# Kernel optimization log

Measured on AMD Instinct MI355X. Metric: run time of the kernel, lower is better.

Reference implementation:

```python
import jax, jax.numpy as jnp
import numpy as np

B = 4096       # batch of instance features
N = 131072     # num_samples (cluster memory slots)
D = 256        # num_features
TEMP = 0.05
EPS = 1e-12    # F.normalize eps


def setup_inputs() -> dict:
    key = jax.random.key(0)
    k1, k2, k3 = jax.random.split(key, 3)
    inputs = jax.random.normal(k1, (B, D), dtype=jnp.float32)
    targets = jax.random.randint(k2, (B,), 0, N, dtype=jnp.int64)
    # learned/buffer memory bank; original registers zeros but is populated with
    # L2-normalized cluster centroids before use -> initialize likewise
    feats = jax.random.normal(k3, (N, D), dtype=jnp.float32)
    feats = feats / jnp.linalg.norm(feats, axis=1, keepdims=True)
    feature_memory = jnp.zeros((1,), dtype=jnp.float32)  # unused by forward
    return {"inputs": inputs, "targets": targets, "feature_memory": feature_memory,
            "k": 10, "features": feats}


def reference(inputs, targets, feature_memory, k, features):
    # inputs: [B, D], targets: [B] int, features: [N, D]
    # F.normalize(inputs, dim=1)
    nrm = jnp.linalg.norm(inputs, axis=1, keepdims=True)
    x = inputs / jnp.maximum(nrm, EPS)
    # CM_Hard forward output: x @ features.T  (the per-cluster argmin loop has
    # no effect on the forward output; it only drives the buffer EMA in backward)
    logits = jnp.matmul(x, features.T) / TEMP          # [B, N]
    # F.cross_entropy(logits, targets), mean reduction
    lse = jax.nn.logsumexp(logits, axis=1)             # [B]
    tgt_logit = jnp.take_along_axis(logits, targets[:, None].astype(jnp.int32), axis=1)[:, 0]
    loss = jnp.mean(lse - tgt_logit)
    return loss
```

## Files before the change

### kernel.cpp

```cpp
#include <hip/hip_runtime.h>
#include <hip/hip_bf16.h>


typedef __attribute__((ext_vector_type(8))) short bf16x8;
typedef __attribute__((ext_vector_type(4))) float f32x4;
typedef __attribute__((address_space(1))) unsigned int u32g;
typedef __attribute__((address_space(3))) unsigned int u32l;

#define B_ROWS   4096
#define N_FEATS  131072
#define D_DIM    256
#define SCALE_B2 28.853900817779268f
#define LN2F     0.69314718055994531f

#define BM 128
#define BN 128
#define BKT 64
#define NCHUNK 32
#define COLS_PB (N_FEATS / NCHUNK)
#define NTILES  (COLS_PB / BN)
#define TILE_B  (BN * BKT * 2)
#define NSLICE  (NCHUNK * 4)

#define E2(x) __builtin_amdgcn_exp2f(x)

static __device__ __forceinline__ unsigned short f2bf(float x) {
    __hip_bfloat16 h = __float2bfloat16(x);
    return __builtin_bit_cast(unsigned short, h);
}
static __device__ __forceinline__ float bf2f(unsigned short u) {
    return __builtin_bit_cast(float, ((unsigned int)u) << 16);
}

__global__ __launch_bounds__(64) void k_normalize(const float* __restrict__ in,
                                                  unsigned short* __restrict__ xb) {
    const int row  = blockIdx.x;
    const int lane = threadIdx.x;
    float4 v = *(const float4*)(in + (size_t)row * D_DIM + lane * 4);
    float ss = v.x * v.x + v.y * v.y + v.z * v.z + v.w * v.w;
#pragma unroll
    for (int mask = 1; mask < 64; mask <<= 1) ss += __shfl_xor(ss, mask);
    const float sc = SCALE_B2 / fmaxf(sqrtf(ss), 1e-12f);
    ushort4 o;
    o.x = f2bf(v.x * sc); o.y = f2bf(v.y * sc);
    o.z = f2bf(v.z * sc); o.w = f2bf(v.w * sc);
    *(ushort4*)(xb + (size_t)row * D_DIM + lane * 4) = o;
}

__global__ __launch_bounds__(256) void k_cvt_feats(const float* __restrict__ f,
                                                   unsigned short* __restrict__ fb) {
    const int total4 = N_FEATS * D_DIM / 4;
    const int stride = gridDim.x * blockDim.x;
    for (int i = blockIdx.x * blockDim.x + threadIdx.x; i < total4; i += stride) {
        float4 v = ((const float4*)f)[i];
        ushort4 o;
        o.x = f2bf(v.x); o.y = f2bf(v.y); o.z = f2bf(v.z); o.w = f2bf(v.w);
        ((ushort4*)fb)[i] = o;
    }
}

#define STAGE(t_, buf_) do {                                                          \
        const int nt_ = (t_) >> 2, kt_ = (t_) & 3;                                    \
        const unsigned short* s_ = fb + (nbase + (size_t)nt_ * BN) * D_DIM + kt_ * BKT; \
        char* d_ = &Bs[(buf_) * TILE_B + dBase];                                      \
        __builtin_amdgcn_global_load_lds((const u32g*)(s_ + e0), (u32l*)d_, 16, 0, 0);\
        __builtin_amdgcn_global_load_lds((const u32g*)(s_ + e1), (u32l*)(d_ + 8192), 16, 0, 0); \
    } while (0)

#define COMPUTE(ktL, bufL) do {                                                       \
        const char* buf_ = &Bs[(bufL) * TILE_B];                                      \
        bf16x8 bfr[2][2];                                                             \
        _Pragma("unroll")                                                             \
        for (int ks2 = 0; ks2 < 2; ++ks2)                                             \
        _Pragma("unroll")                                                             \
            for (int n = 0; n < 2; ++n) {                                             \
                const int col = wc * 32 + n * 16 + l15;                               \
                const int off = (col * 128 + ks2 * 64 + l4 * 16) ^ ((col & 7) << 4);  \
                bfr[ks2][n] = *(const bf16x8*)(buf_ + off);                           \
            }                                                                         \
        __builtin_amdgcn_s_setprio(1);                                                \
        _Pragma("unroll")                                                             \
        for (int ks2 = 0; ks2 < 2; ++ks2)                                             \
        _Pragma("unroll")                                                             \
            for (int m = 0; m < 4; ++m)                                               \
        _Pragma("unroll")                                                             \
                for (int n = 0; n < 2; ++n)                                           \
                    acc[m][n] = __builtin_amdgcn_mfma_f32_16x16x32_bf16(              \
                        afr[m][(ktL) * 2 + ks2], bfr[ks2][n], acc[m][n], 0, 0, 0);    \
        __builtin_amdgcn_s_setprio(0);                                                \
    } while (0)

#define EPI() do {                                                                    \
        _Pragma("unroll")                                                             \
        for (int m = 0; m < 4; ++m)                                                   \
        _Pragma("unroll")                                                             \
            for (int j = 0; j < 4; ++j) {                                             \
                const int r = m * 4 + j;                                              \
                s_run[r] += E2(acc[m][0][j]) + E2(acc[m][1][j]);                      \
            }                                                                         \
        _Pragma("unroll")                                                             \
        for (int m = 0; m < 4; ++m)                                                   \
        _Pragma("unroll")                                                             \
            for (int n = 0; n < 2; ++n) acc[m][n] = (f32x4){0.f, 0.f, 0.f, 0.f};      \
    } while (0)

#define LOADCVT(t_) do {                                                              \
        const int nt_ = (t_) >> 2, kt_ = (t_) & 3;                                    \
        const float* s0_ = featf + (nbase + (size_t)nt_ * BN + fc0) * D_DIM + kt_ * BKT + fk0; \
        const float* s1_ = featf + (nbase + (size_t)nt_ * BN + fc1) * D_DIM + kt_ * BKT + fk1; \
        float4 a0 = *(const float4*)s0_, a1 = *(const float4*)(s0_ + 4);              \
        float4 b0 = *(const float4*)s1_, b1 = *(const float4*)(s1_ + 4);              \
        unsigned short ua[8] = {f2bf(a0.x), f2bf(a0.y), f2bf(a0.z), f2bf(a0.w),       \
                                f2bf(a1.x), f2bf(a1.y), f2bf(a1.z), f2bf(a1.w)};      \
        unsigned short ub[8] = {f2bf(b0.x), f2bf(b0.y), f2bf(b0.z), f2bf(b0.w),       \
                                f2bf(b1.x), f2bf(b1.y), f2bf(b1.z), f2bf(b1.w)};      \
        ra = *(int4*)ua; rb = *(int4*)ub;                                             \
    } while (0)
#define WRITEB(buf_) do {                                                             \
        char* d_ = &Bs[(buf_) * TILE_B];                                              \
        *(int4*)(d_ + wo0) = ra;                                                      \
        *(int4*)(d_ + wo1) = rb;                                                      \
    } while (0)

template <bool BF16B>
__global__ __launch_bounds__(512, 2) void k_lse_gemm(
    const unsigned short* __restrict__ xb,
    const float* __restrict__ featf,
    const unsigned short* __restrict__ fb,
    float* __restrict__ partials)
{
    __shared__ char Bs[4 * TILE_B];

    const int hw  = blockIdx.y * 32 + blockIdx.x;
    const int lid = (hw & 7) * 128 + (hw >> 3);
    const int bx  = lid & 31;
    const int by  = lid >> 5;

    const int tid  = threadIdx.x;
    const int lane = tid & 63;
    const int w    = tid >> 6;
    const int wr   = w >> 2;
    const int wc   = w & 3;
    const int l15  = lane & 15;
    const int l4   = lane >> 4;

    const int brow     = bx * BM;
    const size_t nbase = (size_t)by * COLS_PB;

    bf16x8 afr[4][8];
#pragma unroll
    for (int m = 0; m < 4; ++m) {
        const unsigned short* ap =
            xb + (size_t)(brow + wr * 64 + m * 16 + l15) * D_DIM + l4 * 8;
#pragma unroll
        for (int ks = 0; ks < 8; ++ks)
            afr[m][ks] = *(const bf16x8*)(ap + ks * 32);
    }

    f32x4 acc[4][2];
#pragma unroll
    for (int m = 0; m < 4; ++m)
#pragma unroll
        for (int n = 0; n < 2; ++n) acc[m][n] = (f32x4){0.f, 0.f, 0.f, 0.f};
    float s_run[16];
#pragma unroll
    for (int r = 0; r < 16; ++r) s_run[r] = 0.f;

    if (BF16B) {
        int e0, e1;
        {
            const int p0 = w * 1024 + lane * 16;
            const int c0 = p0 >> 7;
            e0 = c0 * D_DIM + ((((p0 ^ ((c0 & 7) << 4)) >> 4) & 7) * 8);
            const int p1 = p0 + 8192;
            const int c1 = p1 >> 7;
            e1 = c1 * D_DIM + ((((p1 ^ ((c1 & 7) << 4)) >> 4) & 7) * 8);
        }
        const int dBase = w * 1024;

        STAGE(0, 0);
        STAGE(1, 1);
        for (int nt = 0; nt < NTILES; ++nt) {
            STAGE(nt * 4 + 2, 2);
            asm volatile("s_waitcnt vmcnt(4)\ns_barrier" ::: "memory");
            COMPUTE(0, 0);
            STAGE(nt * 4 + 3, 3);
            asm volatile("s_waitcnt vmcnt(4)\ns_barrier" ::: "memory");
            COMPUTE(1, 1);
            if (nt < NTILES - 1) {
                STAGE(nt * 4 + 4, 0);
                asm volatile("s_waitcnt vmcnt(4)\ns_barrier" ::: "memory");
            } else {
                asm volatile("s_waitcnt vmcnt(2)\ns_barrier" ::: "memory");
            }
            COMPUTE(2, 2);
            if (nt < NTILES - 1) {
                STAGE(nt * 4 + 5, 1);
                asm volatile("s_waitcnt vmcnt(4)\ns_barrier" ::: "memory");
            } else {
                asm volatile("s_waitcnt vmcnt(0)\ns_barrier" ::: "memory");
            }
            COMPUTE(3, 3);
            EPI();
        }
    } else {
        const int c0 = tid, c1 = tid + 512;
        const int fc0 = c0 >> 3, fk0 = (c0 & 7) * 8;
        const int fc1 = c1 >> 3, fk1 = (c1 & 7) * 8;
        const int wo0 = (fc0 * 128 + fk0 * 2) ^ ((fc0 & 7) << 4);
        const int wo1 = (fc1 * 128 + fk1 * 2) ^ ((fc1 & 7) << 4);
        int4 ra, rb;
        LOADCVT(0); WRITEB(0);
        __syncthreads();
        for (int nt = 0; nt < NTILES; ++nt) {
            { LOADCVT(nt * 4 + 1); COMPUTE(0, 0); WRITEB(1); __syncthreads(); }
            { LOADCVT(nt * 4 + 2); COMPUTE(1, 1); WRITEB(0); __syncthreads(); }
            { LOADCVT(nt * 4 + 3); COMPUTE(2, 0); WRITEB(1); __syncthreads(); }
            {
                if (nt < NTILES - 1) LOADCVT(nt * 4 + 4);
                COMPUTE(3, 1);
                EPI();
                if (nt < NTILES - 1) { WRITEB(0); }
                __syncthreads();
            }
        }
    }

#pragma unroll
    for (int r = 0; r < 16; ++r) {
        float S = s_run[r];
#pragma unroll
        for (int mask = 1; mask < 16; mask <<= 1) S += __shfl_xor(S, mask);
        s_run[r] = S;
    }
    if (l15 == 0) {
        const int slice = by * 4 + wc;
#pragma unroll
        for (int r = 0; r < 16; ++r) {
            const int m = r >> 2, j = r & 3;
            const int row = brow + wr * 64 + m * 16 + l4 * 4 + j;
            partials[(size_t)row * NSLICE + slice] = s_run[r];
        }
    }
}

__global__ __launch_bounds__(64) void k_finalize(const float* __restrict__ partials,
                                                 const unsigned short* __restrict__ xb,
                                                 const float* __restrict__ feats,
                                                 const int* __restrict__ targets,
                                                 float* __restrict__ loss) {
    const int row  = blockIdx.x;
    const int lane = threadIdx.x;
    float S = partials[(size_t)row * NSLICE + lane]
            + partials[(size_t)row * NSLICE + 64 + lane];

    const int t = targets[row];
    ushort4 xv = *(const ushort4*)(xb + (size_t)row * D_DIM + lane * 4);
    float4  fv = *(const float4*)(feats + (size_t)t * D_DIM + lane * 4);
    float dot = bf2f(xv.x) * fv.x + bf2f(xv.y) * fv.y +
                bf2f(xv.z) * fv.z + bf2f(xv.w) * fv.w;
#pragma unroll
    for (int mask = 1; mask < 64; mask <<= 1) {
        S   += __shfl_xor(S, mask);
        dot += __shfl_xor(dot, mask);
    }
    if (lane == 0) loss[row] = LN2F * (__builtin_amdgcn_logf(S) - dot);
}

__global__ __launch_bounds__(256) void k_reduce(const float* __restrict__ loss,
                                                float* __restrict__ out) {
    __shared__ float sm[4];
    const int tid = threadIdx.x;
    float s = 0.f;
    for (int i = tid; i < B_ROWS; i += 256) s += loss[i];
#pragma unroll
    for (int mask = 1; mask < 64; mask <<= 1) s += __shfl_xor(s, mask);
    if ((tid & 63) == 0) sm[tid >> 6] = s;
    __syncthreads();
    if (tid == 0) out[0] = (sm[0] + sm[1] + sm[2] + sm[3]) * (1.0f / B_ROWS);
}

extern "C" void kernel_launch(void* const* d_in, const int* in_sizes, int n_in,
                              void* d_out, int out_size, void* d_ws, size_t ws_size,
                              hipStream_t stream) {
    const float* inputs  = (const float*)d_in[0];
    const int*   targets = (const int*)d_in[1];
    const float* feats   = (const float*)d_in[4];
    float* out = (float*)d_out;

    char* ws = (char*)d_ws;
    const size_t off_xb       = 0;
    const size_t off_partials = off_xb + (size_t)B_ROWS * D_DIM * 2;
    const size_t off_loss     = off_partials + (size_t)B_ROWS * NSLICE * sizeof(float);
    const size_t off_fb       = off_loss + (size_t)B_ROWS * sizeof(float);
    const size_t need_fb      = off_fb + (size_t)N_FEATS * D_DIM * 2;

    unsigned short* xb = (unsigned short*)(ws + off_xb);
    float* partials    = (float*)(ws + off_partials);
    float* loss        = (float*)(ws + off_loss);
    unsigned short* fb = (unsigned short*)(ws + off_fb);
    const bool precvt  = ws_size >= need_fb;

    k_normalize<<<B_ROWS, 64, 0, stream>>>(inputs, xb);
    if (precvt) {
        k_cvt_feats<<<2048, 256, 0, stream>>>(feats, fb);
        k_lse_gemm<true><<<dim3(32, NCHUNK), 512, 0, stream>>>(xb, feats, fb, partials);
    } else {
        k_lse_gemm<false><<<dim3(32, NCHUNK), 512, 0, stream>>>(xb, feats, fb, partials);
    }
    k_finalize<<<B_ROWS, 64, 0, stream>>>(partials, xb, feats, targets, loss);
    k_reduce<<<1, 256, 0, stream>>>(loss, out);
}
```

Baseline: 285.9 us.

## Widen GEMM N-tile to 256 and cut column chunks to 8

Doubles the per-block N tile from 128 to 256 columns. Each wave now computes a 64x64 output tile, so every loaded A fragment feeds twice as many MFMAs. The column chunk count drops from 32 to 8, giving fewer partial slices for the finalize kernel, and the block swizzle becomes a simple row/column split. The trade-offs are doubled LDS use (4 buffers of 32KB, 128KB per block), twice the accumulator registers, and possibly lower occupancy under launch_bounds(512,2).

```diff
diff --git a/kernel.cpp b/kernel.cpp
--- a/kernel.cpp
+++ b/kernel.cpp
@@ -14,9 +14,9 @@
 #define LN2F     0.69314718055994531f
 
 #define BM 128
-#define BN 128
+#define BN 256
 #define BKT 64
-#define NCHUNK 32
+#define NCHUNK 8
 #define COLS_PB (N_FEATS / NCHUNK)
 #define NTILES  (COLS_PB / BN)
 #define TILE_B  (BN * BKT * 2)
@@ -65,16 +65,18 @@
         char* d_ = &Bs[(buf_) * TILE_B + dBase];                                      \
         __builtin_amdgcn_global_load_lds((const u32g*)(s_ + e0), (u32l*)d_, 16, 0, 0);\
         __builtin_amdgcn_global_load_lds((const u32g*)(s_ + e1), (u32l*)(d_ + 8192), 16, 0, 0); \
+        __builtin_amdgcn_global_load_lds((const u32g*)(s_ + e2), (u32l*)(d_ + 16384), 16, 0, 0); \
+        __builtin_amdgcn_global_load_lds((const u32g*)(s_ + e3), (u32l*)(d_ + 24576), 16, 0, 0); \
     } while (0)
 
 #define COMPUTE(ktL, bufL) do {                                                       \
         const char* buf_ = &Bs[(bufL) * TILE_B];                                      \
-        bf16x8 bfr[2][2];                                                             \
+        bf16x8 bfr[2][4];                                                             \
         _Pragma("unroll")                                                             \
         for (int ks2 = 0; ks2 < 2; ++ks2)                                             \
         _Pragma("unroll")                                                             \
-            for (int n = 0; n < 2; ++n) {                                             \
-                const int col = wc * 32 + n * 16 + l15;                               \
+            for (int n = 0; n < 4; ++n) {                                             \
+                const int col = wc * 64 + n * 16 + l15;                               \
                 const int off = (col * 128 + ks2 * 64 + l4 * 16) ^ ((col & 7) << 4);  \
                 bfr[ks2][n] = *(const bf16x8*)(buf_ + off);                           \
             }                                                                         \
@@ -84,7 +86,7 @@
         _Pragma("unroll")                                                             \
             for (int m = 0; m < 4; ++m)                                               \
         _Pragma("unroll")                                                             \
-                for (int n = 0; n < 2; ++n)                                           \
+                for (int n = 0; n < 4; ++n)                                           \
                     acc[m][n] = __builtin_amdgcn_mfma_f32_16x16x32_bf16(              \
                         afr[m][(ktL) * 2 + ks2], bfr[ks2][n], acc[m][n], 0, 0, 0);    \
         __builtin_amdgcn_s_setprio(0);                                                \
@@ -96,30 +98,32 @@
         _Pragma("unroll")                                                             \
             for (int j = 0; j < 4; ++j) {                                             \
                 const int r = m * 4 + j;                                              \
-                s_run[r] += E2(acc[m][0][j]) + E2(acc[m][1][j]);                      \
+                s_run[r] += (E2(acc[m][0][j]) + E2(acc[m][1][j]))                     \
+                          + (E2(acc[m][2][j]) + E2(acc[m][3][j]));                    \
             }                                                                         \
         _Pragma("unroll")                                                             \
         for (int m = 0; m < 4; ++m)                                                   \
         _Pragma("unroll")                                                             \
-            for (int n = 0; n < 2; ++n) acc[m][n] = (f32x4){0.f, 0.f, 0.f, 0.f};      \
-    } while (0)
-
-#define LOADCVT(t_) do {                                                              \
-        const int nt_ = (t_) >> 2, kt_ = (t_) & 3;                                    \
-        const float* s0_ = featf + (nbase + (size_t)nt_ * BN + fc0) * D_DIM + kt_ * BKT + fk0; \
-        const float* s1_ = featf + (nbase + (size_t)nt_ * BN + fc1) * D_DIM + kt_ * BKT + fk1; \
-        float4 a0 = *(const float4*)s0_, a1 = *(const float4*)(s0_ + 4);              \
-        float4 b0 = *(const float4*)s1_, b1 = *(const float4*)(s1_ + 4);              \
-        unsigned short ua[8] = {f2bf(a0.x), f2bf(a0.y), f2bf(a0.z), f2bf(a0.w),       \
-                                f2bf(a1.x), f2bf(a1.y), f2bf(a1.z), f2bf(a1.w)};      \
-        unsigned short ub[8] = {f2bf(b0.x), f2bf(b0.y), f2bf(b0.z), f2bf(b0.w),       \
-                                f2bf(b1.x), f2bf(b1.y), f2bf(b1.z), f2bf(b1.w)};      \
-        ra = *(int4*)ua; rb = *(int4*)ub;                                             \
-    } while (0)
+            for (int n = 0; n < 4; ++n) acc[m][n] = (f32x4){0.f, 0.f, 0.f, 0.f};      \
+    } while (0)
+
+#define LOADCVT1(q_, t_, r_) do {                                                     \
+        const int cc_ = tid + (q_) * 512;                                             \
+        const int col_ = cc_ >> 3, k_ = (cc_ & 7) * 8;                                \
+        const float* s_ = featf + (nbase + (size_t)((t_) >> 2) * BN + col_) * D_DIM   \
+                          + ((t_) & 3) * BKT + k_;                                    \
+        float4 f0 = *(const float4*)s_;                                               \
+        float4 f1 = *(const float4*)(s_ + 4);                                         \
+        unsigned short u_[8] = {f2bf(f0.x), f2bf(f0.y), f2bf(f0.z), f2bf(f0.w),       \
+                                f2bf(f1.x), f2bf(f1.y), f2bf(f1.z), f2bf(f1.w)};      \
+        r_ = *(int4*)u_;                                                              \
+    } while (0)
+#define LOADCVT(t_) do { LOADCVT1(0, t_, ra); LOADCVT1(1, t_, rb);                    \
+                         LOADCVT1(2, t_, rc); LOADCVT1(3, t_, rd); } while (0)
 #define WRITEB(buf_) do {                                                             \
         char* d_ = &Bs[(buf_) * TILE_B];                                              \
-        *(int4*)(d_ + wo0) = ra;                                                      \
-        *(int4*)(d_ + wo1) = rb;                                                      \
+        *(int4*)(d_ + wo0) = ra; *(int4*)(d_ + wo1) = rb;                             \
+        *(int4*)(d_ + wo2) = rc; *(int4*)(d_ + wo3) = rd;                             \
     } while (0)
 
 template <bool BF16B>
@@ -132,9 +136,8 @@
     __shared__ char Bs[4 * TILE_B];
 
     const int hw  = blockIdx.y * 32 + blockIdx.x;
-    const int lid = (hw & 7) * 128 + (hw >> 3);
-    const int bx  = lid & 31;
-    const int by  = lid >> 5;
+    const int bx  = hw >> 3;
+    const int by  = hw & 7;
 
     const int tid  = threadIdx.x;
     const int lane = tid & 63;
@@ -157,17 +160,17 @@
             afr[m][ks] = *(const bf16x8*)(ap + ks * 32);
     }
 
-    f32x4 acc[4][2];
+    f32x4 acc[4][4];
 #pragma unroll
     for (int m = 0; m < 4; ++m)
 #pragma unroll
-        for (int n = 0; n < 2; ++n) acc[m][n] = (f32x4){0.f, 0.f, 0.f, 0.f};
+        for (int n = 0; n < 4; ++n) acc[m][n] = (f32x4){0.f, 0.f, 0.f, 0.f};
     float s_run[16];
 #pragma unroll
     for (int r = 0; r < 16; ++r) s_run[r] = 0.f;
 
     if (BF16B) {
-        int e0, e1;
+        int e0, e1, e2, e3;
         {
             const int p0 = w * 1024 + lane * 16;
             const int c0 = p0 >> 7;
@@ -175,6 +178,12 @@
             const int p1 = p0 + 8192;
             const int c1 = p1 >> 7;
             e1 = c1 * D_DIM + ((((p1 ^ ((c1 & 7) << 4)) >> 4) & 7) * 8);
+            const int p2 = p0 + 16384;
+            const int c2 = p2 >> 7;
+            e2 = c2 * D_DIM + ((((p2 ^ ((c2 & 7) << 4)) >> 4) & 7) * 8);
+            const int p3 = p0 + 24576;
+            const int c3 = p3 >> 7;
+            e3 = c3 * D_DIM + ((((p3 ^ ((c3 & 7) << 4)) >> 4) & 7) * 8);
         }
         const int dBase = w * 1024;
 
@@ -182,21 +191,21 @@
         STAGE(1, 1);
         for (int nt = 0; nt < NTILES; ++nt) {
             STAGE(nt * 4 + 2, 2);
-            asm volatile("s_waitcnt vmcnt(4)\ns_barrier" ::: "memory");
+            asm volatile("s_waitcnt vmcnt(8)\ns_barrier" ::: "memory");
             COMPUTE(0, 0);
             STAGE(nt * 4 + 3, 3);
-            asm volatile("s_waitcnt vmcnt(4)\ns_barrier" ::: "memory");
+            asm volatile("s_waitcnt vmcnt(8)\ns_barrier" ::: "memory");
             COMPUTE(1, 1);
             if (nt < NTILES - 1) {
                 STAGE(nt * 4 + 4, 0);
+                asm volatile("s_waitcnt vmcnt(8)\ns_barrier" ::: "memory");
+            } else {
                 asm volatile("s_waitcnt vmcnt(4)\ns_barrier" ::: "memory");
-            } else {
-                asm volatile("s_waitcnt vmcnt(2)\ns_barrier" ::: "memory");
             }
             COMPUTE(2, 2);
             if (nt < NTILES - 1) {
                 STAGE(nt * 4 + 5, 1);
-                asm volatile("s_waitcnt vmcnt(4)\ns_barrier" ::: "memory");
+                asm volatile("s_waitcnt vmcnt(8)\ns_barrier" ::: "memory");
             } else {
                 asm volatile("s_waitcnt vmcnt(0)\ns_barrier" ::: "memory");
             }
@@ -204,12 +213,15 @@
             EPI();
         }
     } else {
-        const int c0 = tid, c1 = tid + 512;
-        const int fc0 = c0 >> 3, fk0 = (c0 & 7) * 8;
-        const int fc1 = c1 >> 3, fk1 = (c1 & 7) * 8;
-        const int wo0 = (fc0 * 128 + fk0 * 2) ^ ((fc0 & 7) << 4);
-        const int wo1 = (fc1 * 128 + fk1 * 2) ^ ((fc1 & 7) << 4);
-        int4 ra, rb;
+        const int cc0 = tid;
+        const int wo0 = (((cc0 >> 3) * 128 + (cc0 & 7) * 16)) ^ (((cc0 >> 3) & 7) << 4);
+        const int cc1 = tid + 512;
+        const int wo1 = (((cc1 >> 3) * 128 + (cc1 & 7) * 16)) ^ (((cc1 >> 3) & 7) << 4);
+        const int cc2 = tid + 1024;
+        const int wo2 = (((cc2 >> 3) * 128 + (cc2 & 7) * 16)) ^ (((cc2 >> 3) & 7) << 4);
+        const int cc3 = tid + 1536;
+        const int wo3 = (((cc3 >> 3) * 128 + (cc3 & 7) * 16)) ^ (((cc3 >> 3) & 7) << 4);
+        int4 ra, rb, rc, rd;
         LOADCVT(0); WRITEB(0);
         __syncthreads();
         for (int nt = 0; nt < NTILES; ++nt) {
@@ -251,8 +263,7 @@
                                                  float* __restrict__ loss) {
     const int row  = blockIdx.x;
     const int lane = threadIdx.x;
-    float S = partials[(size_t)row * NSLICE + lane]
-            + partials[(size_t)row * NSLICE + 64 + lane];
+    float S = (lane < NSLICE) ? partials[(size_t)row * NSLICE + lane] : 0.0f;
 
     const int t = targets[row];
     ushort4 xv = *(const ushort4*)(xb + (size_t)row * D_DIM + lane * 4);
```

Result: slower. 494.5 us (+73.0%).

## Enlarge GEMM tile to 256x256 with LDS-staged A and B double buffering

Applied to the files above, without the earlier changes.

Grows the LSE-GEMM block tile from 128x128 to 256x256 and halves the N chunks. A is now streamed through LDS alongside B instead of being held in registers, using 128 KB of dynamic shared memory in two ping-pong buffers with loads interleaved between the MFMA quadrants. Each block does more math per byte loaded, which cuts global/L2 traffic, but occupancy drops to one block per CU and the accumulator register footprint roughly doubles. The finalize kernel is updated to the new partial-slice count.

```diff
diff --git a/kernel.cpp b/kernel.cpp
--- a/kernel.cpp
+++ b/kernel.cpp
@@ -13,13 +13,15 @@
 #define SCALE_B2 28.853900817779268f
 #define LN2F     0.69314718055994531f
 
-#define BM 128
-#define BN 128
+#define BM 256
+#define BN 256
 #define BKT 64
-#define NCHUNK 32
+#define NCHUNK 16
 #define COLS_PB (N_FEATS / NCHUNK)
 #define NTILES  (COLS_PB / BN)
-#define TILE_B  (BN * BKT * 2)
+#define TT      (NTILES * 4)
+#define HBUF    16384
+#define BUFSZ   32768
 #define NSLICE  (NCHUNK * 4)
 
 #define E2(x) __builtin_amdgcn_exp2f(x)
@@ -59,82 +61,89 @@
     }
 }
 
-#define STAGE(t_, buf_) do {                                                          \
-        const int nt_ = (t_) >> 2, kt_ = (t_) & 3;                                    \
-        const unsigned short* s_ = fb + (nbase + (size_t)nt_ * BN) * D_DIM + kt_ * BKT; \
-        char* d_ = &Bs[(buf_) * TILE_B + dBase];                                      \
-        __builtin_amdgcn_global_load_lds((const u32g*)(s_ + e0), (u32l*)d_, 16, 0, 0);\
-        __builtin_amdgcn_global_load_lds((const u32g*)(s_ + e1), (u32l*)(d_ + 8192), 16, 0, 0); \
-    } while (0)
-
-#define COMPUTE(ktL, bufL) do {                                                       \
-        const char* buf_ = &Bs[(bufL) * TILE_B];                                      \
-        bf16x8 bfr[2][2];                                                             \
+#define GL(src_, dst_) __builtin_amdgcn_global_load_lds((const u32g*)(src_), (u32l*)(dst_), 16, 0, 0)
+
+#define STG_A(Tn_, P_, h_) do { if ((Tn_) < TT) {                                     \
+        const unsigned short* s_ = xb + (size_t)(brow + (h_) * 128) * D_DIM + ((Tn_) & 3) * BKT; \
+        char* d_ = As + (P_) * BUFSZ + (h_) * HBUF + dBase;                           \
+        GL(s_ + E0v, d_); GL(s_ + E1v, d_ + 8192); } } while (0)
+#define STG_B(Tn_, P_, h_) do { if ((Tn_) < TT) {                                     \
+        const unsigned short* s_ = fb + (nbase + (size_t)((Tn_) >> 2) * BN + (h_) * 128) * D_DIM + ((Tn_) & 3) * BKT; \
+        char* d_ = Bsm + (P_) * BUFSZ + (h_) * HBUF + dBase;                          \
+        GL(s_ + E0v, d_); GL(s_ + E1v, d_ + 8192); } } while (0)
+
+#define RD_A(P_, mh_) do {                                                            \
+        const char* ab_ = As + (P_) * BUFSZ + (mh_) * 8192;                           \
+        _Pragma("unroll")                                                             \
+        for (int mf = 0; mf < 4; ++mf)                                                \
+        _Pragma("unroll")                                                             \
+            for (int ks2 = 0; ks2 < 2; ++ks2)                                         \
+                afr[mf][ks2] = *(const bf16x8*)(ab_ + aOff[mf][ks2]);                 \
+    } while (0)
+#define RD_B(P_, nh_) do {                                                            \
+        const char* bb_ = Bsm + (P_) * BUFSZ + (nh_) * 4096;                          \
+        _Pragma("unroll")                                                             \
+        for (int nf = 0; nf < 2; ++nf)                                                \
+        _Pragma("unroll")                                                             \
+            for (int ks2 = 0; ks2 < 2; ++ks2)                                         \
+                bfr[nf][ks2] = *(const bf16x8*)(bb_ + bOff[nf][ks2]);                 \
+    } while (0)
+
+#define MM(mh_, nh_, ZC_) do {                                                        \
+        __builtin_amdgcn_s_setprio(1);                                                \
         _Pragma("unroll")                                                             \
         for (int ks2 = 0; ks2 < 2; ++ks2)                                             \
         _Pragma("unroll")                                                             \
-            for (int n = 0; n < 2; ++n) {                                             \
-                const int col = wc * 32 + n * 16 + l15;                               \
-                const int off = (col * 128 + ks2 * 64 + l4 * 16) ^ ((col & 7) << 4);  \
-                bfr[ks2][n] = *(const bf16x8*)(buf_ + off);                           \
-            }                                                                         \
-        __builtin_amdgcn_s_setprio(1);                                                \
-        _Pragma("unroll")                                                             \
-        for (int ks2 = 0; ks2 < 2; ++ks2)                                             \
-        _Pragma("unroll")                                                             \
-            for (int m = 0; m < 4; ++m)                                               \
-        _Pragma("unroll")                                                             \
-                for (int n = 0; n < 2; ++n)                                           \
-                    acc[m][n] = __builtin_amdgcn_mfma_f32_16x16x32_bf16(              \
-                        afr[m][(ktL) * 2 + ks2], bfr[ks2][n], acc[m][n], 0, 0, 0);    \
+            for (int mf = 0; mf < 4; ++mf)                                            \
+        _Pragma("unroll")                                                             \
+                for (int nf = 0; nf < 2; ++nf) {                                      \
+                    const f32x4 cin_ = ((ZC_) && ks2 == 0) ? (f32x4){0.f, 0.f, 0.f, 0.f} \
+                                                           : acc[(mh_) * 4 + mf][(nh_) * 2 + nf]; \
+                    acc[(mh_) * 4 + mf][(nh_) * 2 + nf] =                             \
+                        __builtin_amdgcn_mfma_f32_16x16x32_bf16(                      \
+                            afr[mf][ks2], bfr[nf][ks2], cin_, 0, 0, 0);               \
+                }                                                                     \
         __builtin_amdgcn_s_setprio(0);                                                \
     } while (0)
 
+#define KT(ktL, ZCL, t4_) do {                                                        \
+        asm volatile("s_waitcnt vmcnt(0)\ns_barrier" ::: "memory");                   \
+        RD_A((ktL) & 1, 0); RD_B((ktL) & 1, 0);                                       \
+        STG_A((t4_) + (ktL) + 1, ((ktL) + 1) & 1, 0);                                 \
+        STG_A((t4_) + (ktL) + 1, ((ktL) + 1) & 1, 1);                                 \
+        MM(0, 0, ZCL);                                                                \
+        RD_B((ktL) & 1, 1);                                                           \
+        STG_B((t4_) + (ktL) + 1, ((ktL) + 1) & 1, 0);                                 \
+        STG_B((t4_) + (ktL) + 1, ((ktL) + 1) & 1, 1);                                 \
+        MM(0, 1, ZCL);                                                                \
+        RD_A((ktL) & 1, 1); RD_B((ktL) & 1, 0); MM(1, 0, ZCL);                        \
+        RD_B((ktL) & 1, 1); MM(1, 1, ZCL);                                            \
+    } while (0)
+
 #define EPI() do {                                                                    \
         _Pragma("unroll")                                                             \
-        for (int m = 0; m < 4; ++m)                                                   \
-        _Pragma("unroll")                                                             \
-            for (int j = 0; j < 4; ++j) {                                             \
-                const int r = m * 4 + j;                                              \
-                s_run[r] += E2(acc[m][0][j]) + E2(acc[m][1][j]);                      \
-            }                                                                         \
-        _Pragma("unroll")                                                             \
-        for (int m = 0; m < 4; ++m)                                                   \
-        _Pragma("unroll")                                                             \
-            for (int n = 0; n < 2; ++n) acc[m][n] = (f32x4){0.f, 0.f, 0.f, 0.f};      \
-    } while (0)
-
-#define LOADCVT(t_) do {                                                              \
-        const int nt_ = (t_) >> 2, kt_ = (t_) & 3;                                    \
-        const float* s0_ = featf + (nbase + (size_t)nt_ * BN + fc0) * D_DIM + kt_ * BKT + fk0; \
-        const float* s1_ = featf + (nbase + (size_t)nt_ * BN + fc1) * D_DIM + kt_ * BKT + fk1; \
-        float4 a0 = *(const float4*)s0_, a1 = *(const float4*)(s0_ + 4);              \
-        float4 b0 = *(const float4*)s1_, b1 = *(const float4*)(s1_ + 4);              \
-        unsigned short ua[8] = {f2bf(a0.x), f2bf(a0.y), f2bf(a0.z), f2bf(a0.w),       \
-                                f2bf(a1.x), f2bf(a1.y), f2bf(a1.z), f2bf(a1.w)};      \
-        unsigned short ub[8] = {f2bf(b0.x), f2bf(b0.y), f2bf(b0.z), f2bf(b0.w),       \
-                                f2bf(b1.x), f2bf(b1.y), f2bf(b1.z), f2bf(b1.w)};      \
-        ra = *(int4*)ua; rb = *(int4*)ub;                                             \
-    } while (0)
-#define WRITEB(buf_) do {                                                             \
-        char* d_ = &Bs[(buf_) * TILE_B];                                              \
-        *(int4*)(d_ + wo0) = ra;                                                      \
-        *(int4*)(d_ + wo1) = rb;                                                      \
+        for (int m = 0; m < 8; ++m)                                                   \
+        _Pragma("unroll")                                                             \
+            for (int j = 0; j < 4; ++j)                                               \
+                s_run[m * 4 + j] += (E2(acc[m][0][j]) + E2(acc[m][1][j]))             \
+                                  + (E2(acc[m][2][j]) + E2(acc[m][3][j]));            \
     } while (0)
 
 template <bool BF16B>
-__global__ __launch_bounds__(512, 2) void k_lse_gemm(
+__global__ __launch_bounds__(512, 1) void k_lse_gemm(
     const unsigned short* __restrict__ xb,
     const float* __restrict__ featf,
     const unsigned short* __restrict__ fb,
     float* __restrict__ partials)
 {
-    __shared__ char Bs[4 * TILE_B];
-
-    const int hw  = blockIdx.y * 32 + blockIdx.x;
-    const int lid = (hw & 7) * 128 + (hw >> 3);
-    const int bx  = lid & 31;
-    const int by  = lid >> 5;
+    extern __shared__ char smem[];
+    char* As  = smem;
+    char* Bsm = smem + 65536;
+
+    const int hw  = blockIdx.y * 16 + blockIdx.x;
+    const int lid = (hw & 7) * 32 + (hw >> 3);
+    const int bx  = lid & 15;
+    const int by  = lid >> 4;
 
     const int tid  = threadIdx.x;
     const int lane = tid & 63;
@@ -142,92 +151,83 @@
     const int wr   = w >> 2;
     const int wc   = w & 3;
     const int l15  = lane & 15;
-    const int l4   = lane >> 4;
+    const int l4q  = lane >> 4;
 
     const int brow     = bx * BM;
     const size_t nbase = (size_t)by * COLS_PB;
 
-    bf16x8 afr[4][8];
-#pragma unroll
-    for (int m = 0; m < 4; ++m) {
-        const unsigned short* ap =
-            xb + (size_t)(brow + wr * 64 + m * 16 + l15) * D_DIM + l4 * 8;
-#pragma unroll
-        for (int ks = 0; ks < 8; ++ks)
-            afr[m][ks] = *(const bf16x8*)(ap + ks * 32);
-    }
-
-    f32x4 acc[4][2];
-#pragma unroll
-    for (int m = 0; m < 4; ++m)
-#pragma unroll
-        for (int n = 0; n < 2; ++n) acc[m][n] = (f32x4){0.f, 0.f, 0.f, 0.f};
-    float s_run[16];
-#pragma unroll
-    for (int r = 0; r < 16; ++r) s_run[r] = 0.f;
+    const int swz = (l15 & 7) << 4;
+    int aOff[4][2], bOff[2][2];
+#pragma unroll
+    for (int mf = 0; mf < 4; ++mf)
+#pragma unroll
+        for (int ks2 = 0; ks2 < 2; ++ks2)
+            aOff[mf][ks2] = (wr * 128 + mf * 16 + l15) * 128 + ((ks2 * 64 + l4q * 16) ^ swz);
+#pragma unroll
+    for (int nf = 0; nf < 2; ++nf)
+#pragma unroll
+        for (int ks2 = 0; ks2 < 2; ++ks2)
+            bOff[nf][ks2] = (wc * 64 + nf * 16 + l15) * 128 + ((ks2 * 64 + l4q * 16) ^ swz);
+
+    int E0v, E1v;
+    {
+        const int p0 = w * 1024 + lane * 16;
+        const int c0 = p0 >> 7;
+        E0v = c0 * D_DIM + ((((p0 ^ ((c0 & 7) << 4)) >> 4) & 7) * 8);
+        const int p1 = p0 + 8192;
+        const int c1 = p1 >> 7;
+        E1v = c1 * D_DIM + ((((p1 ^ ((c1 & 7) << 4)) >> 4) & 7) * 8);
+    }
+    const int dBase = w * 1024;
+
+    bf16x8 afr[4][2];
+    bf16x8 bfr[2][2];
+    f32x4 acc[8][4];
+    float s_run[32];
+#pragma unroll
+    for (int r = 0; r < 32; ++r) s_run[r] = 0.f;
 
     if (BF16B) {
-        int e0, e1;
-        {
-            const int p0 = w * 1024 + lane * 16;
-            const int c0 = p0 >> 7;
-            e0 = c0 * D_DIM + ((((p0 ^ ((c0 & 7) << 4)) >> 4) & 7) * 8);
-            const int p1 = p0 + 8192;
-            const int c1 = p1 >> 7;
-            e1 = c1 * D_DIM + ((((p1 ^ ((c1 & 7) << 4)) >> 4) & 7) * 8);
-        }
-        const int dBase = w * 1024;
-
-        STAGE(0, 0);
-        STAGE(1, 1);
+        STG_A(0, 0, 0); STG_A(0, 0, 1); STG_B(0, 0, 0); STG_B(0, 0, 1);
         for (int nt = 0; nt < NTILES; ++nt) {
-            STAGE(nt * 4 + 2, 2);
-            asm volatile("s_waitcnt vmcnt(4)\ns_barrier" ::: "memory");
-            COMPUTE(0, 0);
-            STAGE(nt * 4 + 3, 3);
-            asm volatile("s_waitcnt vmcnt(4)\ns_barrier" ::: "memory");
-            COMPUTE(1, 1);
-            if (nt < NTILES - 1) {
-                STAGE(nt * 4 + 4, 0);
-                asm volatile("s_waitcnt vmcnt(4)\ns_barrier" ::: "memory");
-            } else {
-                asm volatile("s_waitcnt vmcnt(2)\ns_barrier" ::: "memory");
-            }
-            COMPUTE(2, 2);
-            if (nt < NTILES - 1) {
-                STAGE(nt * 4 + 5, 1);
-                asm volatile("s_waitcnt vmcnt(4)\ns_barrier" ::: "memory");
-            } else {
-                asm volatile("s_waitcnt vmcnt(0)\ns_barrier" ::: "memory");
-            }
-            COMPUTE(3, 3);
+            const int t4 = nt * 4;
+            KT(0, true,  t4);
+            KT(1, false, t4);
+            KT(2, false, t4);
+            KT(3, false, t4);
             EPI();
         }
     } else {
-        const int c0 = tid, c1 = tid + 512;
-        const int fc0 = c0 >> 3, fk0 = (c0 & 7) * 8;
-        const int fc1 = c1 >> 3, fk1 = (c1 & 7) * 8;
-        const int wo0 = (fc0 * 128 + fk0 * 2) ^ ((fc0 & 7) << 4);
-        const int wo1 = (fc1 * 128 + fk1 * 2) ^ ((fc1 & 7) << 4);
-        int4 ra, rb;
-        LOADCVT(0); WRITEB(0);
-        __syncthreads();
         for (int nt = 0; nt < NTILES; ++nt) {
-            { LOADCVT(nt * 4 + 1); COMPUTE(0, 0); WRITEB(1); __syncthreads(); }
-            { LOADCVT(nt * 4 + 2); COMPUTE(1, 1); WRITEB(0); __syncthreads(); }
-            { LOADCVT(nt * 4 + 3); COMPUTE(2, 0); WRITEB(1); __syncthreads(); }
-            {
-                if (nt < NTILES - 1) LOADCVT(nt * 4 + 4);
-                COMPUTE(3, 1);
-                EPI();
-                if (nt < NTILES - 1) { WRITEB(0); }
+            for (int kt = 0; kt < 4; ++kt) {
                 __syncthreads();
+#pragma unroll
+                for (int c = 0; c < 4; ++c) {
+                    const int q   = (tid + c * 512) * 16;
+                    const int row = q >> 7;
+                    const int dst = q ^ ((row & 7) << 4);
+                    const int kel = (q & 127) >> 1;
+                    int4 va = *(const int4*)(xb + (size_t)(brow + row) * D_DIM + kt * BKT + kel);
+                    *(int4*)(As + dst) = va;
+                    const float* sb = featf + (nbase + (size_t)nt * BN + row) * D_DIM + kt * BKT + kel;
+                    float4 f0 = *(const float4*)sb, f1 = *(const float4*)(sb + 4);
+                    unsigned short ub[8] = {f2bf(f0.x), f2bf(f0.y), f2bf(f0.z), f2bf(f0.w),
+                                            f2bf(f1.x), f2bf(f1.y), f2bf(f1.z), f2bf(f1.w)};
+                    *(int4*)(Bsm + dst) = *(int4*)ub;
+                }
+                __syncthreads();
+                const bool zc = (kt == 0);
+                RD_A(0, 0); RD_B(0, 0); MM(0, 0, zc);
+                RD_B(0, 1);             MM(0, 1, zc);
+                RD_A(0, 1); RD_B(0, 0); MM(1, 0, zc);
+                RD_B(0, 1);             MM(1, 1, zc);
             }
+            EPI();
         }
     }
 
 #pragma unroll
-    for (int r = 0; r < 16; ++r) {
+    for (int r = 0; r < 32; ++r) {
         float S = s_run[r];
 #pragma unroll
         for (int mask = 1; mask < 16; mask <<= 1) S += __shfl_xor(S, mask);
@@ -236,9 +236,9 @@
     if (l15 == 0) {
         const int slice = by * 4 + wc;
 #pragma unroll
-        for (int r = 0; r < 16; ++r) {
+        for (int r = 0; r < 32; ++r) {
             const int m = r >> 2, j = r & 3;
-            const int row = brow + wr * 64 + m * 16 + l4 * 4 + j;
+            const int row = brow + wr * 128 + m * 16 + l4q * 4 + j;
             partials[(size_t)row * NSLICE + slice] = s_run[r];
         }
     }
@@ -251,8 +251,7 @@
                                                  float* __restrict__ loss) {
     const int row  = blockIdx.x;
     const int lane = threadIdx.x;
-    float S = partials[(size_t)row * NSLICE + lane]
-            + partials[(size_t)row * NSLICE + 64 + lane];
+    float S = partials[(size_t)row * NSLICE + lane];
 
     const int t = targets[row];
     ushort4 xv = *(const ushort4*)(xb + (size_t)row * D_DIM + lane * 4);
@@ -301,12 +300,21 @@
     unsigned short* fb = (unsigned short*)(ws + off_fb);
     const bool precvt  = ws_size >= need_fb;
 
+    static bool attrib_set = false;
+    if (!attrib_set) {
+        hipFuncSetAttribute((const void*)&k_lse_gemm<true>,
+                            hipFuncAttributeMaxDynamicSharedMemorySize, 131072);
+        hipFuncSetAttribute((const void*)&k_lse_gemm<false>,
+                            hipFuncAttributeMaxDynamicSharedMemorySize, 131072);
+        attrib_set = true;
+    }
+
     k_normalize<<<B_ROWS, 64, 0, stream>>>(inputs, xb);
     if (precvt) {
         k_cvt_feats<<<2048, 256, 0, stream>>>(feats, fb);
-        k_lse_gemm<true><<<dim3(32, NCHUNK), 512, 0, stream>>>(xb, feats, fb, partials);
+        k_lse_gemm<true><<<dim3(16, NCHUNK), 512, 131072, stream>>>(xb, feats, fb, partials);
     } else {
-        k_lse_gemm<false><<<dim3(32, NCHUNK), 512, 0, stream>>>(xb, feats, fb, partials);
+        k_lse_gemm<false><<<dim3(16, NCHUNK), 512, 131072, stream>>>(xb, feats, fb, partials);
     }
     k_finalize<<<B_ROWS, 64, 0, stream>>>(partials, xb, feats, targets, loss);
     k_reduce<<<1, 256, 0, stream>>>(loss, out);
```

New measurement: 398.3 us. 1.39x slower.
